# Kernel tuning notes

Measured on AMD Instinct MI355X. Metric: run time of the kernel, lower is better.

## Reference

```python
import jax, jax.numpy as jnp
import numpy as np

B, LQ, LK, D, H = 2, 1024, 1024, 1024, 16
DH = D // H


def setup_inputs() -> dict:
    key = jax.random.key(0)
    ks = jax.random.split(key, 14)
    s = 1.0 / np.sqrt(D)
    inp = {
        "q": jax.random.normal(ks[0], (B, LQ, D), jnp.float32),
        "k": jax.random.normal(ks[1], (B, LK, D), jnp.float32),
        "v": jax.random.normal(ks[2], (B, LK, D), jnp.float32),
        "Wq": jax.random.normal(ks[3], (D, D), jnp.float32) * s,
        "bq": jnp.zeros((D,), jnp.float32),
        "Wk": jax.random.normal(ks[4], (D, D), jnp.float32) * s,
        "bk": jnp.zeros((D,), jnp.float32),
        "Wv": jax.random.normal(ks[5], (D, D), jnp.float32) * s,
        "bv": jnp.zeros((D,), jnp.float32),
        "Wo": jax.random.normal(ks[6], (D, D), jnp.float32) * s,
        "bo": jnp.zeros((D,), jnp.float32),
        "logits_bias": jax.random.normal(ks[7], (B, LQ, LK), jnp.float32),
        "key_padding_mask": jax.random.randint(ks[8], (B, LK), 0, 2) > 0,
    }
    return inp


def _split_heads(x):
    b, l, _ = x.shape
    return x.reshape(b, l, H, DH).transpose(0, 2, 1, 3)  # [B,H,L,DH]


def reference(q, k, v, Wq, bq, Wk, bk, Wv, bv, Wo, bo, logits_bias, key_padding_mask):
    qh = _split_heads(q @ Wq.T + bq)  # [B,H,Lq,DH]
    kh = _split_heads(k @ Wk.T + bk)  # [B,H,Lk,DH]
    vh = _split_heads(v @ Wv.T + bv)  # [B,H,Lk,DH]

    neg = jnp.finfo(qh.dtype).min
    # attn_mask = logits_bias broadcast over heads, masked_fill at padded keys
    attn_mask = jnp.where(key_padding_mask[:, None, None, :],
                          neg, logits_bias[:, None, :, :])  # [B,1,Lq,Lk]

    scale = 1.0 / np.sqrt(DH)
    scores = jnp.einsum('bhqd,bhkd->bhqk', qh, kh) * scale + attn_mask
    probs = jax.nn.softmax(scores, axis=-1)
    out = jnp.einsum('bhqk,bhkd->bhqd', probs, vh)  # [B,H,Lq,DH]
    out = out.transpose(0, 2, 1, 3).reshape(q.shape[0], q.shape[1], D)
    return out @ Wo.T + bo
```

## Files before the change

### kernel.cpp

```cpp
#include <hip/hip_runtime.h>


typedef _Float16 half8 __attribute__((ext_vector_type(8)));
typedef _Float16 half4_t __attribute__((ext_vector_type(4)));
typedef float f32x4 __attribute__((ext_vector_type(4)));

#define MFMA16(a, b, c) __builtin_amdgcn_mfma_f32_16x16x32_f16((a), (b), (c), 0, 0, 0)

__device__ __forceinline__ void gload16(const void* g, void* l) {
  __builtin_amdgcn_global_load_lds(
      (const __attribute__((address_space(1))) unsigned int*)g,
      (__attribute__((address_space(3))) unsigned int*)l, 16, 0, 0);
}

__device__ __forceinline__ half8 frag_ld(const _Float16* t, int row, int ck) {
  return *(const half8*)(t + row * 64 + (((ck ^ (row & 7)) << 3)));
}

__global__ __launch_bounds__(256) void cvt_f32_f16(
    const float* __restrict__ q, const float* __restrict__ k, const float* __restrict__ v,
    const float* __restrict__ Wq, const float* __restrict__ Wk,
    const float* __restrict__ Wv, const float* __restrict__ Wo,
    _Float16* __restrict__ q16, _Float16* __restrict__ k16, _Float16* __restrict__ v16,
    _Float16* __restrict__ w16) {
  const int y = blockIdx.y;
  if (y >= 3 && blockIdx.x >= 512) return;
  const float* s;
  _Float16* d;
  const size_t M = (size_t)1024 * 1024;
  switch (y) {
    case 0: s = q;  d = q16; break;
    case 1: s = k;  d = k16; break;
    case 2: s = v;  d = v16; break;
    case 3: s = Wq; d = w16; break;
    case 4: s = Wk; d = w16 + M; break;
    case 5: s = Wv; d = w16 + 2 * M; break;
    default: s = Wo; d = w16 + 3 * M; break;
  }
  const size_t i = ((size_t)blockIdx.x * 256 + threadIdx.x) * 8;
  const float4 a = *(const float4*)(s + i);
  const float4 bvv = *(const float4*)(s + i + 4);
  half8 h;
  h[0] = (_Float16)a.x; h[1] = (_Float16)a.y; h[2] = (_Float16)a.z; h[3] = (_Float16)a.w;
  h[4] = (_Float16)bvv.x; h[5] = (_Float16)bvv.y; h[6] = (_Float16)bvv.z; h[7] = (_Float16)bvv.w;
  *(half8*)(d + i) = h;
}

__global__ __launch_bounds__(256) void mm64(
    const _Float16* __restrict__ Aq, const _Float16* __restrict__ Ak,
    const _Float16* __restrict__ Av, const _Float16* __restrict__ W16,
    const float* __restrict__ c0, const float* __restrict__ c1,
    const float* __restrict__ c2, _Float16* __restrict__ Dq,
    _Float16* __restrict__ Dk, _Float16* __restrict__ Dvt,
    float* __restrict__ Df, int is_final) {
  __shared__ __align__(16) _Float16 lds[8192];
  _Float16* As = lds;
  _Float16* Bs = lds + 4096;

  const int tid = threadIdx.x;
  const int wv = tid >> 6, ln = tid & 63;
  const int quad = ln >> 4, col = ln & 15;
  const int wm = wv >> 1, wn = wv & 1;
  const int n0 = blockIdx.x * 64;
  const int m0 = blockIdx.y * 64;
  const int z = blockIdx.z;

  const _Float16* A = (z == 0) ? Aq : (z == 1) ? Ak : Av;
  const _Float16* Bw = W16 + (size_t)z * 1024 * 1024;
  const float* bias = (z == 0) ? c0 : (z == 1) ? c1 : c2;

  const f32x4 zero4 = {0.f, 0.f, 0.f, 0.f};
  f32x4 acc[2][2];
#pragma unroll
  for (int i = 0; i < 2; ++i)
#pragma unroll
    for (int j = 0; j < 2; ++j) acc[i][j] = zero4;

  for (int k0 = 0; k0 < 1024; k0 += 64) {
    __syncthreads();
#pragma unroll
    for (int j = 0; j < 2; ++j) {
      const int ci = j * 256 + wv * 64 + ln;
      const int row = ci >> 3;
      const int lc = (ci & 7) ^ (row & 7);
      gload16(A + (size_t)(m0 + row) * 1024 + k0 + lc * 8,
              As + (size_t)(j * 256 + wv * 64) * 8);
      gload16(Bw + (size_t)(n0 + row) * 1024 + k0 + lc * 8,
              Bs + (size_t)(j * 256 + wv * 64) * 8);
    }
    __syncthreads();
#pragma unroll
    for (int kk = 0; kk < 2; ++kk) {
      half8 af[2], bf[2];
#pragma unroll
      for (int mi = 0; mi < 2; ++mi)
        af[mi] = frag_ld(As, wm * 32 + mi * 16 + col, kk * 4 + quad);
#pragma unroll
      for (int ni = 0; ni < 2; ++ni)
        bf[ni] = frag_ld(Bs, wn * 32 + ni * 16 + col, kk * 4 + quad);
#pragma unroll
      for (int mi = 0; mi < 2; ++mi)
#pragma unroll
        for (int ni = 0; ni < 2; ++ni)
          acc[mi][ni] = MFMA16(af[mi], bf[ni], acc[mi][ni]);
    }
  }

  float bv[2];
#pragma unroll
  for (int ni = 0; ni < 2; ++ni) bv[ni] = bias[n0 + wn * 32 + ni * 16 + col];

  if (is_final) {
#pragma unroll
    for (int mi = 0; mi < 2; ++mi) {
      const int m_g = m0 + wm * 32 + mi * 16 + quad * 4;
#pragma unroll
      for (int ni = 0; ni < 2; ++ni) {
        const int n_g = n0 + wn * 32 + ni * 16 + col;
#pragma unroll
        for (int r = 0; r < 4; ++r)
          Df[(size_t)(m_g + r) * 1024 + n_g] = acc[mi][ni][r] + bv[ni];
      }
    }
  } else if (z < 2) {
    _Float16* D = z ? Dk : Dq;
    const int h = n0 >> 6;
#pragma unroll
    for (int mi = 0; mi < 2; ++mi) {
      const int m_g = m0 + wm * 32 + mi * 16 + quad * 4;
#pragma unroll
      for (int ni = 0; ni < 2; ++ni) {
        const int dh = (wn * 32 + ni * 16 + col);
#pragma unroll
        for (int r = 0; r < 4; ++r) {
          const int b = (m_g + r) >> 10, l = (m_g + r) & 1023;
          D[((size_t)((b * 16 + h) * 1024) + l) * 64 + dh] =
              (_Float16)(acc[mi][ni][r] + bv[ni]);
        }
      }
    }
  } else {
    __syncthreads();
    _Float16* Ct = lds;
#pragma unroll
    for (int mi = 0; mi < 2; ++mi) {
      const int ml = wm * 32 + mi * 16 + quad * 4;
#pragma unroll
      for (int ni = 0; ni < 2; ++ni) {
        const int nl = wn * 32 + ni * 16 + col;
#pragma unroll
        for (int r = 0; r < 4; ++r)
          Ct[(size_t)nl * 80 + ml + r] = (_Float16)(acc[mi][ni][r] + bv[ni]);
      }
    }
    __syncthreads();
    const int h = n0 >> 6;
#pragma unroll
    for (int it = 0; it < 2; ++it) {
      const int ci = it * 256 + tid;
      const int n = ci >> 3;
      const int mc = (ci & 7) * 8;
      const half8 hv = *(const half8*)(Ct + (size_t)n * 80 + mc);
      const int m_g = m0 + mc;
      const int b = m_g >> 10, l = m_g & 1023;
      *(half8*)(Dvt + ((size_t)((b * 16 + h) * 64 + n)) * 1024 + l) = hv;
    }
  }
}

__global__ __launch_bounds__(256) void attn(
    const _Float16* __restrict__ Qh, const _Float16* __restrict__ Kh,
    const _Float16* __restrict__ Vt, const float* __restrict__ biasL,
    const int* __restrict__ kpm, _Float16* __restrict__ AO) {
  __shared__ __align__(16) _Float16 KV[4][4096];
  __shared__ __align__(16) _Float16 Pt[4][1024];

  const int tid = threadIdx.x;
  const int wv = tid >> 6, ln = tid & 63;
  const int quad = ln >> 4, col = ln & 15;
  const int qsub = wv & 1, khalf = wv >> 1;
  const int q0 = blockIdx.x * 32;
  const int bh = blockIdx.y;
  const int b = bh >> 4, hh = bh & 15;
  const int qg = q0 + qsub * 16 + col;

  const _Float16* Qp = Qh + ((size_t)bh * 1024 + qg) * 64;
  const half8 bq0 = *(const half8*)(Qp + quad * 8);
  const half8 bq1 = *(const half8*)(Qp + 32 + quad * 8);

  const f32x4 zero4 = {0.f, 0.f, 0.f, 0.f};
  f32x4 o[4];
#pragma unroll
  for (int ni = 0; ni < 4; ++ni) o[ni] = zero4;
  float m_i = -1e30f, l_i = 0.f;

  _Float16* Pw = Pt[wv];
  const _Float16* Ks = KV[khalf];
  const _Float16* Vs = KV[2 + khalf];
  const float* biasRow = biasL + ((size_t)(b * 1024 + qg)) * 1024;
  const int* kpmRow = kpm + b * 1024;

  const int stage_koff_base = (wv & 1) * 512;

  for (int it = 0; it < 8; ++it) {
    const int koff = khalf * 512 + it * 64;
    const int skoff = stage_koff_base + it * 64;

    __syncthreads();
#pragma unroll
    for (int j = 0; j < 8; ++j) {
      const int ci = j * 64 + ln;
      const int row = ci >> 3;
      const int lc = (ci & 7) ^ (row & 7);
      const void* src =
          (wv < 2) ? (const void*)(Kh + ((size_t)bh * 1024 + skoff + row) * 64 + lc * 8)
                   : (const void*)(Vt + ((size_t)bh * 64 + row) * 1024 + skoff + lc * 8);
      gload16(src, KV[wv] + j * 512);
    }
    f32x4 bb[4];
    int4 mk4[4];
#pragma unroll
    for (int mi = 0; mi < 4; ++mi) {
      const int kg = koff + mi * 16 + quad * 4;
      mk4[mi] = *(const int4*)&kpmRow[kg];
      bb[mi] = *(const f32x4*)&biasRow[kg];
    }
    __syncthreads();

    f32x4 s[4];
#pragma unroll
    for (int mi = 0; mi < 4; ++mi) {
      f32x4 a4 = zero4;
      a4 = MFMA16(frag_ld(Ks, mi * 16 + col, quad), bq0, a4);
      a4 = MFMA16(frag_ld(Ks, mi * 16 + col, 4 + quad), bq1, a4);
      s[mi] = a4;
    }
#pragma unroll
    for (int mi = 0; mi < 4; ++mi) {
      const int* mp = (const int*)&mk4[mi];
#pragma unroll
      for (int r = 0; r < 4; ++r)
        s[mi][r] = mp[r] ? -1e9f : s[mi][r] * 0.125f + bb[mi][r];
    }

    float rm = -1e30f;
#pragma unroll
    for (int mi = 0; mi < 4; ++mi)
#pragma unroll
      for (int r = 0; r < 4; ++r) rm = fmaxf(rm, s[mi][r]);
    rm = fmaxf(rm, __shfl_xor(rm, 16));
    rm = fmaxf(rm, __shfl_xor(rm, 32));
    const float mn = fmaxf(m_i, rm);
    const float alpha = __expf(m_i - mn);
    m_i = mn;
    float ps = 0.f;
#pragma unroll
    for (int mi = 0; mi < 4; ++mi)
#pragma unroll
      for (int r = 0; r < 4; ++r) {
        const float p = __expf(s[mi][r] - mn);
        s[mi][r] = p;
        ps += p;
      }
    ps += __shfl_xor(ps, 16);
    ps += __shfl_xor(ps, 32);
    l_i = l_i * alpha + ps;
#pragma unroll
    for (int ni = 0; ni < 4; ++ni)
#pragma unroll
      for (int r = 0; r < 4; ++r) o[ni][r] *= alpha;

#pragma unroll
    for (int mi = 0; mi < 4; ++mi) {
      half4_t h;
      h[0] = (_Float16)s[mi][0]; h[1] = (_Float16)s[mi][1];
      h[2] = (_Float16)s[mi][2]; h[3] = (_Float16)s[mi][3];
      const int kloc = mi * 16 + quad * 4;
      const int chunk = kloc >> 3;
      *(half4_t*)(Pw + col * 64 + (((chunk ^ (col & 7)) << 3) | (kloc & 7))) = h;
    }
    const half8 p0 = frag_ld(Pw, col, quad);
    const half8 p1 = frag_ld(Pw, col, 4 + quad);

#pragma unroll
    for (int ni = 0; ni < 4; ++ni) {
      o[ni] = MFMA16(frag_ld(Vs, ni * 16 + col, quad), p0, o[ni]);
      o[ni] = MFMA16(frag_ld(Vs, ni * 16 + col, 4 + quad), p1, o[ni]);
    }
  }

  __syncthreads();
  f32x4* Ox = (f32x4*)&Pt[0][0];
  float* MlS = (float*)&KV[0][0];
  if (khalf == 1) {
#pragma unroll
    for (int ni = 0; ni < 4; ++ni) Ox[(qsub * 4 + ni) * 64 + ln] = o[ni];
    MlS[qsub * 64 + ln] = m_i;
    MlS[128 + qsub * 64 + ln] = l_i;
  }
  __syncthreads();
  if (khalf == 0) {
    const float m2 = MlS[qsub * 64 + ln];
    const float l2 = MlS[128 + qsub * 64 + ln];
    const float ms = fmaxf(m_i, m2);
    const float w1 = __expf(m_i - ms);
    const float w2 = __expf(m2 - ms);
    const float inv = 1.0f / (l_i * w1 + l2 * w2);
#pragma unroll
    for (int ni = 0; ni < 4; ++ni) {
      const f32x4 o2 = Ox[(qsub * 4 + ni) * 64 + ln];
      half4_t h;
#pragma unroll
      for (int r = 0; r < 4; ++r)
        h[r] = (_Float16)((o[ni][r] * w1 + o2[r] * w2) * inv);
      *(half4_t*)&AO[((size_t)(b * 1024 + qg)) * 1024 + hh * 64 + ni * 16 + quad * 4] = h;
    }
  }
}

extern "C" void kernel_launch(void* const* d_in, const int* in_sizes, int n_in,
                              void* d_out, int out_size, void* d_ws, size_t ws_size,
                              hipStream_t stream) {
  (void)in_sizes; (void)n_in; (void)out_size; (void)ws_size;
  const float* q = (const float*)d_in[0];
  const float* k = (const float*)d_in[1];
  const float* v = (const float*)d_in[2];
  const float* Wq = (const float*)d_in[3];
  const float* bq = (const float*)d_in[4];
  const float* Wk = (const float*)d_in[5];
  const float* bk = (const float*)d_in[6];
  const float* Wv = (const float*)d_in[7];
  const float* bv = (const float*)d_in[8];
  const float* Wo = (const float*)d_in[9];
  const float* bo = (const float*)d_in[10];
  const float* lb = (const float*)d_in[11];
  const int* kpm = (const int*)d_in[12];
  float* out = (float*)d_out;

  const size_t NT = (size_t)2 * 1024 * 1024;
  _Float16* q16 = (_Float16*)d_ws;
  _Float16* k16 = q16 + NT;
  _Float16* v16 = k16 + NT;
  _Float16* Qh = v16 + NT;
  _Float16* Kh = Qh + NT;
  _Float16* Vt = Kh + NT;
  _Float16* w16 = Vt + NT;
  _Float16* AO = q16;

  cvt_f32_f16<<<dim3(1024, 7), 256, 0, stream>>>(q, k, v, Wq, Wk, Wv, Wo,
                                                 q16, k16, v16, w16);
  mm64<<<dim3(16, 32, 3), 256, 0, stream>>>(q16, k16, v16, w16, bq, bk, bv,
                                            Qh, Kh, Vt, nullptr, 0);
  attn<<<dim3(32, 32), 256, 0, stream>>>(Qh, Kh, Vt, lb, kpm, AO);
  mm64<<<dim3(16, 32, 1), 256, 0, stream>>>(AO, nullptr, nullptr, w16 + 3 * NT / 2,
                                            bo, nullptr, nullptr, nullptr, nullptr,
                                            nullptr, out, 1);
}
```

Measured before the change: 186.1 us.

## Double-buffer GEMM and attention LDS tiles with raw waitcnt barriers; widen GEMM N tile

Both the projection GEMM and the attention kernel now stage the next K tile (and the next bias/mask registers) into a second LDS buffer while computing on the current one. They synchronise with explicit vmcnt/lgkmcnt waits and raw s_barrier instead of __syncthreads. The GEMM tile is widened from 64x64 to 64x128, which raises per-block MFMA work and halves the grid. The aim is to hide global-load latency behind compute, at the cost of more LDS per block and hand-counted wait values that must match the number of loads issued.

```diff
diff --git a/kernel.cpp b/kernel.cpp
--- a/kernel.cpp
+++ b/kernel.cpp
@@ -6,6 +6,10 @@
 typedef float f32x4 __attribute__((ext_vector_type(4)));
 
 #define MFMA16(a, b, c) __builtin_amdgcn_mfma_f32_16x16x32_f16((a), (b), (c), 0, 0, 0)
+
+#define WAITCNT_VM(n) asm volatile("s_waitcnt vmcnt(" #n ")" ::: "memory")
+#define WAITCNT_LGKM0() asm volatile("s_waitcnt lgkmcnt(0)" ::: "memory")
+#define RAW_BARRIER() asm volatile("s_barrier" ::: "memory")
 
 __device__ __forceinline__ void gload16(const void* g, void* l) {
   __builtin_amdgcn_global_load_lds(
@@ -46,22 +50,20 @@
   *(half8*)(d + i) = h;
 }
 
-__global__ __launch_bounds__(256) void mm64(
+__global__ __launch_bounds__(256) void mmp(
     const _Float16* __restrict__ Aq, const _Float16* __restrict__ Ak,
     const _Float16* __restrict__ Av, const _Float16* __restrict__ W16,
     const float* __restrict__ c0, const float* __restrict__ c1,
     const float* __restrict__ c2, _Float16* __restrict__ Dq,
     _Float16* __restrict__ Dk, _Float16* __restrict__ Dvt,
     float* __restrict__ Df, int is_final) {
-  __shared__ __align__(16) _Float16 lds[8192];
-  _Float16* As = lds;
-  _Float16* Bs = lds + 4096;
+  __shared__ __align__(16) _Float16 lds[24576];
 
   const int tid = threadIdx.x;
   const int wv = tid >> 6, ln = tid & 63;
   const int quad = ln >> 4, col = ln & 15;
   const int wm = wv >> 1, wn = wv & 1;
-  const int n0 = blockIdx.x * 64;
+  const int n0 = blockIdx.x * 128;
   const int m0 = blockIdx.y * 64;
   const int z = blockIdx.z;
 
@@ -69,54 +71,90 @@
   const _Float16* Bw = W16 + (size_t)z * 1024 * 1024;
   const float* bias = (z == 0) ? c0 : (z == 1) ? c1 : c2;
 
+  auto stage = [&](int buf, int k0) {
+#pragma unroll
+    for (int j = 0; j < 6; ++j) {
+      const int ci = j * 256 + tid;
+      const _Float16* src;
+      if (ci < 512) {
+        const int row = ci >> 3, lc = (ci & 7) ^ (row & 7);
+        src = A + (size_t)(m0 + row) * 1024 + k0 + lc * 8;
+      } else {
+        const int di = ci - 512;
+        const int row = di >> 3, lc = (di & 7) ^ (row & 7);
+        src = Bw + (size_t)(n0 + row) * 1024 + k0 + lc * 8;
+      }
+      gload16(src, lds + buf * 12288 + (j * 256 + wv * 64) * 8);
+    }
+  };
+
   const f32x4 zero4 = {0.f, 0.f, 0.f, 0.f};
-  f32x4 acc[2][2];
+  f32x4 acc[2][4];
 #pragma unroll
   for (int i = 0; i < 2; ++i)
 #pragma unroll
-    for (int j = 0; j < 2; ++j) acc[i][j] = zero4;
-
-  for (int k0 = 0; k0 < 1024; k0 += 64) {
-    __syncthreads();
-#pragma unroll
-    for (int j = 0; j < 2; ++j) {
-      const int ci = j * 256 + wv * 64 + ln;
-      const int row = ci >> 3;
-      const int lc = (ci & 7) ^ (row & 7);
-      gload16(A + (size_t)(m0 + row) * 1024 + k0 + lc * 8,
-              As + (size_t)(j * 256 + wv * 64) * 8);
-      gload16(Bw + (size_t)(n0 + row) * 1024 + k0 + lc * 8,
-              Bs + (size_t)(j * 256 + wv * 64) * 8);
-    }
-    __syncthreads();
+    for (int j = 0; j < 4; ++j) acc[i][j] = zero4;
+
+  stage(0, 0);
+  for (int i = 0; i < 15; ++i) {
+    stage((i + 1) & 1, (i + 1) * 64);
+    WAITCNT_VM(6);
+    RAW_BARRIER();
+    const _Float16* As = lds + (i & 1) * 12288;
+    const _Float16* Bs = As + 4096;
+    half8 af[2][2], bf[2][4];
 #pragma unroll
     for (int kk = 0; kk < 2; ++kk) {
-      half8 af[2], bf[2];
+#pragma unroll
+      for (int mi = 0; mi < 2; ++mi)
+        af[kk][mi] = frag_ld(As, wm * 32 + mi * 16 + col, kk * 4 + quad);
+#pragma unroll
+      for (int ni = 0; ni < 4; ++ni)
+        bf[kk][ni] = frag_ld(Bs, wn * 64 + ni * 16 + col, kk * 4 + quad);
+    }
+    WAITCNT_LGKM0();
+    RAW_BARRIER();
+#pragma unroll
+    for (int kk = 0; kk < 2; ++kk)
+#pragma unroll
+      for (int mi = 0; mi < 2; ++mi)
+#pragma unroll
+        for (int ni = 0; ni < 4; ++ni)
+          acc[mi][ni] = MFMA16(af[kk][mi], bf[kk][ni], acc[mi][ni]);
+  }
+  {
+    WAITCNT_VM(0);
+    RAW_BARRIER();
+    const _Float16* As = lds + 12288;
+    const _Float16* Bs = As + 4096;
+#pragma unroll
+    for (int kk = 0; kk < 2; ++kk) {
+      half8 af[2], bf[4];
 #pragma unroll
       for (int mi = 0; mi < 2; ++mi)
         af[mi] = frag_ld(As, wm * 32 + mi * 16 + col, kk * 4 + quad);
 #pragma unroll
-      for (int ni = 0; ni < 2; ++ni)
-        bf[ni] = frag_ld(Bs, wn * 32 + ni * 16 + col, kk * 4 + quad);
+      for (int ni = 0; ni < 4; ++ni)
+        bf[ni] = frag_ld(Bs, wn * 64 + ni * 16 + col, kk * 4 + quad);
 #pragma unroll
       for (int mi = 0; mi < 2; ++mi)
 #pragma unroll
-        for (int ni = 0; ni < 2; ++ni)
+        for (int ni = 0; ni < 4; ++ni)
           acc[mi][ni] = MFMA16(af[mi], bf[ni], acc[mi][ni]);
     }
   }
 
-  float bv[2];
-#pragma unroll
-  for (int ni = 0; ni < 2; ++ni) bv[ni] = bias[n0 + wn * 32 + ni * 16 + col];
+  float bv[4];
+#pragma unroll
+  for (int ni = 0; ni < 4; ++ni) bv[ni] = bias[n0 + wn * 64 + ni * 16 + col];
 
   if (is_final) {
 #pragma unroll
     for (int mi = 0; mi < 2; ++mi) {
       const int m_g = m0 + wm * 32 + mi * 16 + quad * 4;
 #pragma unroll
-      for (int ni = 0; ni < 2; ++ni) {
-        const int n_g = n0 + wn * 32 + ni * 16 + col;
+      for (int ni = 0; ni < 4; ++ni) {
+        const int n_g = n0 + wn * 64 + ni * 16 + col;
 #pragma unroll
         for (int r = 0; r < 4; ++r)
           Df[(size_t)(m_g + r) * 1024 + n_g] = acc[mi][ni][r] + bv[ni];
@@ -124,13 +162,13 @@
     }
   } else if (z < 2) {
     _Float16* D = z ? Dk : Dq;
-    const int h = n0 >> 6;
 #pragma unroll
     for (int mi = 0; mi < 2; ++mi) {
       const int m_g = m0 + wm * 32 + mi * 16 + quad * 4;
 #pragma unroll
-      for (int ni = 0; ni < 2; ++ni) {
-        const int dh = (wn * 32 + ni * 16 + col);
+      for (int ni = 0; ni < 4; ++ni) {
+        const int n_g = n0 + wn * 64 + ni * 16 + col;
+        const int h = n_g >> 6, dh = n_g & 63;
 #pragma unroll
         for (int r = 0; r < 4; ++r) {
           const int b = (m_g + r) >> 10, l = (m_g + r) & 1023;
@@ -146,24 +184,25 @@
     for (int mi = 0; mi < 2; ++mi) {
       const int ml = wm * 32 + mi * 16 + quad * 4;
 #pragma unroll
-      for (int ni = 0; ni < 2; ++ni) {
-        const int nl = wn * 32 + ni * 16 + col;
+      for (int ni = 0; ni < 4; ++ni) {
+        const int nl = wn * 64 + ni * 16 + col;
 #pragma unroll
         for (int r = 0; r < 4; ++r)
-          Ct[(size_t)nl * 80 + ml + r] = (_Float16)(acc[mi][ni][r] + bv[ni]);
+          Ct[(size_t)nl * 72 + ml + r] = (_Float16)(acc[mi][ni][r] + bv[ni]);
       }
     }
     __syncthreads();
-    const int h = n0 >> 6;
-#pragma unroll
-    for (int it = 0; it < 2; ++it) {
+#pragma unroll
+    for (int it = 0; it < 4; ++it) {
       const int ci = it * 256 + tid;
       const int n = ci >> 3;
       const int mc = (ci & 7) * 8;
-      const half8 hv = *(const half8*)(Ct + (size_t)n * 80 + mc);
+      const half8 hv = *(const half8*)(Ct + (size_t)n * 72 + mc);
+      const int n_g = n0 + n;
+      const int h = n_g >> 6, dh = n_g & 63;
       const int m_g = m0 + mc;
       const int b = m_g >> 10, l = m_g & 1023;
-      *(half8*)(Dvt + ((size_t)((b * 16 + h) * 64 + n)) * 1024 + l) = hv;
+      *(half8*)(Dvt + ((size_t)((b * 16 + h) * 64 + dh)) * 1024 + l) = hv;
     }
   }
 }
@@ -172,7 +211,7 @@
     const _Float16* __restrict__ Qh, const _Float16* __restrict__ Kh,
     const _Float16* __restrict__ Vt, const float* __restrict__ biasL,
     const int* __restrict__ kpm, _Float16* __restrict__ AO) {
-  __shared__ __align__(16) _Float16 KV[4][4096];
+  __shared__ __align__(16) _Float16 KV[2 * 16384];
   __shared__ __align__(16) _Float16 Pt[4][1024];
 
   const int tid = threadIdx.x;
@@ -187,26 +226,14 @@
   const _Float16* Qp = Qh + ((size_t)bh * 1024 + qg) * 64;
   const half8 bq0 = *(const half8*)(Qp + quad * 8);
   const half8 bq1 = *(const half8*)(Qp + 32 + quad * 8);
-
-  const f32x4 zero4 = {0.f, 0.f, 0.f, 0.f};
-  f32x4 o[4];
-#pragma unroll
-  for (int ni = 0; ni < 4; ++ni) o[ni] = zero4;
-  float m_i = -1e30f, l_i = 0.f;
-
-  _Float16* Pw = Pt[wv];
-  const _Float16* Ks = KV[khalf];
-  const _Float16* Vs = KV[2 + khalf];
+  WAITCNT_VM(0);
+
   const float* biasRow = biasL + ((size_t)(b * 1024 + qg)) * 1024;
   const int* kpmRow = kpm + b * 1024;
-
-  const int stage_koff_base = (wv & 1) * 512;
-
-  for (int it = 0; it < 8; ++it) {
-    const int koff = khalf * 512 + it * 64;
-    const int skoff = stage_koff_base + it * 64;
-
-    __syncthreads();
+  const int stage_kbase = (wv & 1) * 512;
+
+  auto stageKV = [&](int buf, int it) {
+    const int skoff = stage_kbase + it * 64;
 #pragma unroll
     for (int j = 0; j < 8; ++j) {
       const int ci = j * 64 + ln;
@@ -215,18 +242,29 @@
       const void* src =
           (wv < 2) ? (const void*)(Kh + ((size_t)bh * 1024 + skoff + row) * 64 + lc * 8)
                    : (const void*)(Vt + ((size_t)bh * 64 + row) * 1024 + skoff + lc * 8);
-      gload16(src, KV[wv] + j * 512);
-    }
-    f32x4 bb[4];
-    int4 mk4[4];
+      gload16(src, KV + buf * 16384 + wv * 4096 + j * 512);
+    }
+  };
+  auto loadBias = [&](int it, f32x4* bb, int4* mk) {
+    const int koff = khalf * 512 + it * 64;
 #pragma unroll
     for (int mi = 0; mi < 4; ++mi) {
       const int kg = koff + mi * 16 + quad * 4;
-      mk4[mi] = *(const int4*)&kpmRow[kg];
+      mk[mi] = *(const int4*)&kpmRow[kg];
       bb[mi] = *(const f32x4*)&biasRow[kg];
     }
-    __syncthreads();
-
+  };
+
+  const f32x4 zero4 = {0.f, 0.f, 0.f, 0.f};
+  f32x4 o[4];
+#pragma unroll
+  for (int ni = 0; ni < 4; ++ni) o[ni] = zero4;
+  float m_i = -1e30f, l_i = 0.f;
+  _Float16* Pw = Pt[wv];
+
+  auto compute = [&](int buf, const f32x4* bb, const int4* mk) {
+    const _Float16* Ks = KV + buf * 16384 + khalf * 4096;
+    const _Float16* Vs = KV + buf * 16384 + (2 + khalf) * 4096;
     f32x4 s[4];
 #pragma unroll
     for (int mi = 0; mi < 4; ++mi) {
@@ -237,12 +275,11 @@
     }
 #pragma unroll
     for (int mi = 0; mi < 4; ++mi) {
-      const int* mp = (const int*)&mk4[mi];
+      const int* mp = (const int*)&mk[mi];
 #pragma unroll
       for (int r = 0; r < 4; ++r)
         s[mi][r] = mp[r] ? -1e9f : s[mi][r] * 0.125f + bb[mi][r];
     }
-
     float rm = -1e30f;
 #pragma unroll
     for (int mi = 0; mi < 4; ++mi)
@@ -269,7 +306,6 @@
     for (int ni = 0; ni < 4; ++ni)
 #pragma unroll
       for (int r = 0; r < 4; ++r) o[ni][r] *= alpha;
-
 #pragma unroll
     for (int mi = 0; mi < 4; ++mi) {
       half4_t h;
@@ -281,17 +317,35 @@
     }
     const half8 p0 = frag_ld(Pw, col, quad);
     const half8 p1 = frag_ld(Pw, col, 4 + quad);
-
 #pragma unroll
     for (int ni = 0; ni < 4; ++ni) {
       o[ni] = MFMA16(frag_ld(Vs, ni * 16 + col, quad), p0, o[ni]);
       o[ni] = MFMA16(frag_ld(Vs, ni * 16 + col, 4 + quad), p1, o[ni]);
     }
-  }
+  };
+
+  f32x4 bbA[4], bbB[4];
+  int4 mkA[4], mkB[4];
+  stageKV(0, 0);
+  loadBias(0, bbA, mkA);
+  for (int i = 0; i < 7; ++i) {
+    stageKV((i + 1) & 1, i + 1);
+    loadBias(i + 1, bbB, mkB);
+    WAITCNT_VM(16);
+    RAW_BARRIER();
+    compute(i & 1, bbA, mkA);
+    WAITCNT_LGKM0();
+    RAW_BARRIER();
+#pragma unroll
+    for (int mi = 0; mi < 4; ++mi) { bbA[mi] = bbB[mi]; mkA[mi] = mkB[mi]; }
+  }
+  WAITCNT_VM(0);
+  RAW_BARRIER();
+  compute(1, bbA, mkA);
 
   __syncthreads();
   f32x4* Ox = (f32x4*)&Pt[0][0];
-  float* MlS = (float*)&KV[0][0];
+  float* MlS = (float*)&KV[0];
   if (khalf == 1) {
 #pragma unroll
     for (int ni = 0; ni < 4; ++ni) Ox[(qsub * 4 + ni) * 64 + ln] = o[ni];
@@ -349,10 +403,10 @@
 
   cvt_f32_f16<<<dim3(1024, 7), 256, 0, stream>>>(q, k, v, Wq, Wk, Wv, Wo,
                                                  q16, k16, v16, w16);
-  mm64<<<dim3(16, 32, 3), 256, 0, stream>>>(q16, k16, v16, w16, bq, bk, bv,
-                                            Qh, Kh, Vt, nullptr, 0);
+  mmp<<<dim3(8, 32, 3), 256, 0, stream>>>(q16, k16, v16, w16, bq, bk, bv,
+                                          Qh, Kh, Vt, nullptr, 0);
   attn<<<dim3(32, 32), 256, 0, stream>>>(Qh, Kh, Vt, lb, kpm, AO);
-  mm64<<<dim3(16, 32, 1), 256, 0, stream>>>(AO, nullptr, nullptr, w16 + 3 * NT / 2,
-                                            bo, nullptr, nullptr, nullptr, nullptr,
-                                            nullptr, out, 1);
-}
+  mmp<<<dim3(8, 32, 1), 256, 0, stream>>>(AO, nullptr, nullptr, w16 + 3 * NT / 2,
+                                          bo, nullptr, nullptr, nullptr, nullptr,
+                                          nullptr, out, 1);
+}
```

Result: faster. 180.3 us (-3.1%).

## Widen GEMM tile to 64x128 and split K across two wave groups

Applied to the files above, without the earlier changes.

The projection GEMM kernel now computes a 64x128 output tile per block with 512 threads. The two halves of K are handled by separate groups of four waves, and the partial sums are reduced through LDS before the epilogue. This gives more data reuse per loaded A tile and more MFMAs per wave, at the cost of an extra LDS reduction, more LDS per block, and half as many blocks. The final output-projection GEMM grid drops to 256 blocks, which may underfill the GPU.

```diff
diff --git a/kernel.cpp b/kernel.cpp
--- a/kernel.cpp
+++ b/kernel.cpp
@@ -46,124 +46,165 @@
   *(half8*)(d + i) = h;
 }
 
-__global__ __launch_bounds__(256) void mm64(
+__global__ __launch_bounds__(512, 6) void mm8(
     const _Float16* __restrict__ Aq, const _Float16* __restrict__ Ak,
     const _Float16* __restrict__ Av, const _Float16* __restrict__ W16,
     const float* __restrict__ c0, const float* __restrict__ c1,
     const float* __restrict__ c2, _Float16* __restrict__ Dq,
     _Float16* __restrict__ Dk, _Float16* __restrict__ Dvt,
     float* __restrict__ Df, int is_final) {
-  __shared__ __align__(16) _Float16 lds[8192];
-  _Float16* As = lds;
-  _Float16* Bs = lds + 4096;
+  __shared__ __align__(16) _Float16 lds[25600];
 
   const int tid = threadIdx.x;
   const int wv = tid >> 6, ln = tid & 63;
   const int quad = ln >> 4, col = ln & 15;
-  const int wm = wv >> 1, wn = wv & 1;
-  const int n0 = blockIdx.x * 64;
+  const int khalf = wv >> 2, lw = wv & 3;
+  const int wm = lw >> 1, wn = lw & 1;
+  const int n0 = blockIdx.x * 128;
   const int m0 = blockIdx.y * 64;
   const int z = blockIdx.z;
+  const int kbase = khalf * 512;
 
   const _Float16* A = (z == 0) ? Aq : (z == 1) ? Ak : Av;
   const _Float16* Bw = W16 + (size_t)z * 1024 * 1024;
   const float* bias = (z == 0) ? c0 : (z == 1) ? c1 : c2;
 
+  _Float16* As = lds + khalf * 12288;
+  _Float16* Bs = As + 4096;
+
   const f32x4 zero4 = {0.f, 0.f, 0.f, 0.f};
-  f32x4 acc[2][2];
+  f32x4 acc[2][4];
 #pragma unroll
   for (int i = 0; i < 2; ++i)
 #pragma unroll
-    for (int j = 0; j < 2; ++j) acc[i][j] = zero4;
-
-  for (int k0 = 0; k0 < 1024; k0 += 64) {
-    __syncthreads();
-#pragma unroll
-    for (int j = 0; j < 2; ++j) {
-      const int ci = j * 256 + wv * 64 + ln;
-      const int row = ci >> 3;
-      const int lc = (ci & 7) ^ (row & 7);
-      gload16(A + (size_t)(m0 + row) * 1024 + k0 + lc * 8,
-              As + (size_t)(j * 256 + wv * 64) * 8);
-      gload16(Bw + (size_t)(n0 + row) * 1024 + k0 + lc * 8,
-              Bs + (size_t)(j * 256 + wv * 64) * 8);
+    for (int j = 0; j < 4; ++j) acc[i][j] = zero4;
+
+  for (int it = 0; it < 8; ++it) {
+    const int k0 = kbase + it * 64;
+    __syncthreads();
+#pragma unroll
+    for (int j = 0; j < 6; ++j) {
+      const int ci = j * 256 + lw * 64 + ln;
+      const _Float16* src;
+      if (ci < 512) {
+        const int row = ci >> 3, lc = (ci & 7) ^ (row & 7);
+        src = A + (size_t)(m0 + row) * 1024 + k0 + lc * 8;
+      } else {
+        const int di = ci - 512;
+        const int row = di >> 3, lc = (di & 7) ^ (row & 7);
+        src = Bw + (size_t)(n0 + row) * 1024 + k0 + lc * 8;
+      }
+      gload16(src, As + (size_t)(j * 256 + lw * 64) * 8);
     }
     __syncthreads();
 #pragma unroll
     for (int kk = 0; kk < 2; ++kk) {
-      half8 af[2], bf[2];
+      half8 af[2], bf[4];
 #pragma unroll
       for (int mi = 0; mi < 2; ++mi)
         af[mi] = frag_ld(As, wm * 32 + mi * 16 + col, kk * 4 + quad);
 #pragma unroll
-      for (int ni = 0; ni < 2; ++ni)
-        bf[ni] = frag_ld(Bs, wn * 32 + ni * 16 + col, kk * 4 + quad);
+      for (int ni = 0; ni < 4; ++ni)
+        bf[ni] = frag_ld(Bs, wn * 64 + ni * 16 + col, kk * 4 + quad);
 #pragma unroll
       for (int mi = 0; mi < 2; ++mi)
 #pragma unroll
-        for (int ni = 0; ni < 2; ++ni)
+        for (int ni = 0; ni < 4; ++ni)
           acc[mi][ni] = MFMA16(af[mi], bf[ni], acc[mi][ni]);
     }
   }
 
-  float bv[2];
-#pragma unroll
-  for (int ni = 0; ni < 2; ++ni) bv[ni] = bias[n0 + wn * 32 + ni * 16 + col];
-
-  if (is_final) {
-#pragma unroll
-    for (int mi = 0; mi < 2; ++mi) {
-      const int m_g = m0 + wm * 32 + mi * 16 + quad * 4;
-#pragma unroll
-      for (int ni = 0; ni < 2; ++ni) {
-        const int n_g = n0 + wn * 32 + ni * 16 + col;
+  __syncthreads();
+  float* Macc = (float*)lds;
+  if (khalf == 1) {
+#pragma unroll
+    for (int mi = 0; mi < 2; ++mi)
+#pragma unroll
+      for (int ni = 0; ni < 4; ++ni) {
+        const int ml = wm * 32 + mi * 16 + quad * 4;
+        const int nl = wn * 64 + ni * 16 + col;
 #pragma unroll
         for (int r = 0; r < 4; ++r)
-          Df[(size_t)(m_g + r) * 1024 + n_g] = acc[mi][ni][r] + bv[ni];
-      }
-    }
-  } else if (z < 2) {
-    _Float16* D = z ? Dk : Dq;
-    const int h = n0 >> 6;
-#pragma unroll
-    for (int mi = 0; mi < 2; ++mi) {
-      const int m_g = m0 + wm * 32 + mi * 16 + quad * 4;
-#pragma unroll
-      for (int ni = 0; ni < 2; ++ni) {
-        const int dh = (wn * 32 + ni * 16 + col);
-#pragma unroll
-        for (int r = 0; r < 4; ++r) {
-          const int b = (m_g + r) >> 10, l = (m_g + r) & 1023;
-          D[((size_t)((b * 16 + h) * 1024) + l) * 64 + dh] =
-              (_Float16)(acc[mi][ni][r] + bv[ni]);
+          Macc[(size_t)(ml + r) * 128 + nl] = acc[mi][ni][r];
+      }
+  }
+  __syncthreads();
+  if (khalf == 0) {
+#pragma unroll
+    for (int mi = 0; mi < 2; ++mi)
+#pragma unroll
+      for (int ni = 0; ni < 4; ++ni) {
+        const int ml = wm * 32 + mi * 16 + quad * 4;
+        const int nl = wn * 64 + ni * 16 + col;
+#pragma unroll
+        for (int r = 0; r < 4; ++r)
+          acc[mi][ni][r] += Macc[(size_t)(ml + r) * 128 + nl];
+      }
+  }
+
+  float bv[4];
+#pragma unroll
+  for (int ni = 0; ni < 4; ++ni) bv[ni] = bias[n0 + wn * 64 + ni * 16 + col];
+
+  if (z == 2 && !is_final) {
+    _Float16* Ct = lds + 16384;
+    if (khalf == 0) {
+#pragma unroll
+      for (int mi = 0; mi < 2; ++mi)
+#pragma unroll
+        for (int ni = 0; ni < 4; ++ni) {
+          const int ml = wm * 32 + mi * 16 + quad * 4;
+          const int nl = wn * 64 + ni * 16 + col;
+#pragma unroll
+          for (int r = 0; r < 4; ++r)
+            Ct[(size_t)nl * 72 + ml + r] = (_Float16)(acc[mi][ni][r] + bv[ni]);
         }
-      }
-    }
-  } else {
-    __syncthreads();
-    _Float16* Ct = lds;
-#pragma unroll
-    for (int mi = 0; mi < 2; ++mi) {
-      const int ml = wm * 32 + mi * 16 + quad * 4;
-#pragma unroll
-      for (int ni = 0; ni < 2; ++ni) {
-        const int nl = wn * 32 + ni * 16 + col;
-#pragma unroll
-        for (int r = 0; r < 4; ++r)
-          Ct[(size_t)nl * 80 + ml + r] = (_Float16)(acc[mi][ni][r] + bv[ni]);
-      }
-    }
-    __syncthreads();
-    const int h = n0 >> 6;
-#pragma unroll
-    for (int it = 0; it < 2; ++it) {
-      const int ci = it * 256 + tid;
-      const int n = ci >> 3;
-      const int mc = (ci & 7) * 8;
-      const half8 hv = *(const half8*)(Ct + (size_t)n * 80 + mc);
-      const int m_g = m0 + mc;
-      const int b = m_g >> 10, l = m_g & 1023;
-      *(half8*)(Dvt + ((size_t)((b * 16 + h) * 64 + n)) * 1024 + l) = hv;
+    }
+    __syncthreads();
+    if (khalf == 0) {
+#pragma unroll
+      for (int itc = 0; itc < 4; ++itc) {
+        const int ci = itc * 256 + (lw * 64 + ln);
+        const int n = ci >> 3;
+        const int mc = (ci & 7) * 8;
+        const half8 hv = *(const half8*)(Ct + (size_t)n * 72 + mc);
+        const int n_g = n0 + n;
+        const int h = n_g >> 6, dh = n_g & 63;
+        const int m_g = m0 + mc;
+        const int b = m_g >> 10, l = m_g & 1023;
+        *(half8*)(Dvt + ((size_t)((b * 16 + h) * 64 + dh)) * 1024 + l) = hv;
+      }
+    }
+  } else if (khalf == 0) {
+    if (is_final) {
+#pragma unroll
+      for (int mi = 0; mi < 2; ++mi) {
+        const int m_g = m0 + wm * 32 + mi * 16 + quad * 4;
+#pragma unroll
+        for (int ni = 0; ni < 4; ++ni) {
+          const int n_g = n0 + wn * 64 + ni * 16 + col;
+#pragma unroll
+          for (int r = 0; r < 4; ++r)
+            Df[(size_t)(m_g + r) * 1024 + n_g] = acc[mi][ni][r] + bv[ni];
+        }
+      }
+    } else {
+      _Float16* D = z ? Dk : Dq;
+#pragma unroll
+      for (int mi = 0; mi < 2; ++mi) {
+        const int m_g = m0 + wm * 32 + mi * 16 + quad * 4;
+#pragma unroll
+        for (int ni = 0; ni < 4; ++ni) {
+          const int n_g = n0 + wn * 64 + ni * 16 + col;
+          const int h = n_g >> 6, dh = n_g & 63;
+#pragma unroll
+          for (int r = 0; r < 4; ++r) {
+            const int b = (m_g + r) >> 10, l = (m_g + r) & 1023;
+            D[((size_t)((b * 16 + h) * 1024) + l) * 64 + dh] =
+                (_Float16)(acc[mi][ni][r] + bv[ni]);
+          }
+        }
+      }
     }
   }
 }
@@ -349,10 +390,10 @@
 
   cvt_f32_f16<<<dim3(1024, 7), 256, 0, stream>>>(q, k, v, Wq, Wk, Wv, Wo,
                                                  q16, k16, v16, w16);
-  mm64<<<dim3(16, 32, 3), 256, 0, stream>>>(q16, k16, v16, w16, bq, bk, bv,
-                                            Qh, Kh, Vt, nullptr, 0);
+  mm8<<<dim3(8, 32, 3), 512, 0, stream>>>(q16, k16, v16, w16, bq, bk, bv,
+                                          Qh, Kh, Vt, nullptr, 0);
   attn<<<dim3(32, 32), 256, 0, stream>>>(Qh, Kh, Vt, lb, kpm, AO);
-  mm64<<<dim3(16, 32, 1), 256, 0, stream>>>(AO, nullptr, nullptr, w16 + 3 * NT / 2,
-                                            bo, nullptr, nullptr, nullptr, nullptr,
-                                            nullptr, out, 1);
-}
+  mm8<<<dim3(8, 32, 1), 512, 0, stream>>>(AO, nullptr, nullptr, w16 + 3 * NT / 2,
+                                          bo, nullptr, nullptr, nullptr, nullptr,
+                                          nullptr, out, 1);
+}
```

Result: faster. 182.5 us (-2.0%).
